# Performance work log

Measured on AMD Instinct MI355X. Metric: run time of the kernel, lower is better.

The kernel has to match this reference:

```python
import jax, jax.numpy as jnp
import numpy as np
from jax import lax

DIM = 192
HEADS = 4
K = 3
PAD = 1


def conv2d(x, w, groups=1, pad=0):
    # x: [B,C,H,W], w: [O, C//groups, kh, kw]
    return lax.conv_general_dilated(
        x, w, window_strides=(1, 1), padding=[(pad, pad), (pad, pad)],
        dimension_numbers=("NCHW", "OIHW", "NCHW"), feature_group_count=groups)


def setup_inputs() -> dict:
    key = jax.random.key(0)
    ks = jax.random.split(key, 8)
    b, c, h, w = 2, DIM, 256, 256
    x = jax.random.normal(ks[0], (b, c, h, w), dtype=jnp.float32)
    y = jax.random.normal(ks[1], (b, c, h, w), dtype=jnp.float32)
    s = 0.05
    qk_w = jax.random.normal(ks[2], (2 * DIM, DIM, 1, 1), dtype=jnp.float32) * s
    qk_dw_w = jax.random.normal(ks[3], (2 * DIM, 1, K, K), dtype=jnp.float32) * s  # depthwise, groups=2*dim
    v_w = jax.random.normal(ks[4], (DIM, DIM, 1, 1), dtype=jnp.float32) * s
    v_dw_w = jax.random.normal(ks[5], (DIM, DIM, K, K), dtype=jnp.float32) * s    # NOTE: not grouped in source
    proj_w = jax.random.normal(ks[6], (DIM, DIM, 1, 1), dtype=jnp.float32) * s
    temperature = jnp.ones((HEADS, 1, 1), dtype=jnp.float32)
    return {"x": x, "y": y, "qk_w": qk_w, "qk_dw_w": qk_dw_w, "v_w": v_w,
            "v_dw_w": v_dw_w, "proj_w": proj_w, "temperature": temperature}


def reference(x, y, qk_w, qk_dw_w, v_w, v_dw_w, proj_w, temperature):
    b, c, h, w = x.shape
    hd = c // HEADS  # channels per head
    qk = conv2d(conv2d(x, qk_w), qk_dw_w, groups=2 * DIM, pad=PAD)  # [b, 2c, h, w]
    q, k = jnp.split(qk, 2, axis=1)
    v = conv2d(conv2d(y, v_w), v_dw_w, pad=PAD)  # full conv (groups=1), per source

    def to_heads(t):
        return t.reshape(b, HEADS, hd, h * w)  # b head c (hw)

    q, k, v = to_heads(q), to_heads(k), to_heads(v)
    # L2 normalize along spatial (last) axis, eps matches torch F.normalize (1e-12)
    q = q / jnp.maximum(jnp.linalg.norm(q, axis=-1, keepdims=True), 1e-12)
    k = k / jnp.maximum(jnp.linalg.norm(k, axis=-1, keepdims=True), 1e-12)
    attn = jnp.einsum("bhcn,bhdn->bhcd", q, k) * temperature  # [b, head, c, c]
    attn = jax.nn.softmax(attn, axis=-1)
    out = jnp.einsum("bhcd,bhdn->bhcn", attn, v)
    out = out.reshape(b, c, h, w)
    return conv2d(out, proj_w)
```

## Files before the change

kernel.cpp:

```cpp
#include <hip/hip_runtime.h>
#include <hip/hip_bf16.h>

#define NPIX 65536
#define CDIM 192
#define C2   384
#define HEADS 4
#define HD   48
#define PROW 258
#define XTROWS (PROW * PROW)

typedef float f32x4 __attribute__((ext_vector_type(4)));
typedef short short8 __attribute__((ext_vector_type(8)));

__device__ __forceinline__ unsigned short f2bf(float x) {
  union { float f; unsigned u; } v; v.f = x;
  unsigned r = v.u + 0x7fff + ((v.u >> 16) & 1);
  return (unsigned short)(r >> 16);
}
__device__ __forceinline__ float bf2f(unsigned short x) {
  union { unsigned u; float f; } v; v.u = ((unsigned)x) << 16;
  return v.f;
}
__device__ __forceinline__ int f4(int r) { return (r ^ (r >> 2)) & 3; }

__device__ __forceinline__ void gload_lds16(const void* g, void* l) {
  __builtin_amdgcn_global_load_lds(
      (const __attribute__((address_space(1))) unsigned int*)g,
      (__attribute__((address_space(3))) unsigned int*)l, 16, 0, 0);
}

__global__ __launch_bounds__(256) void castw_kernel(
    const float* __restrict__ qkw, const float* __restrict__ vw,
    unsigned short* __restrict__ wqk, unsigned short* __restrict__ wv) {
  int i = blockIdx.x * 256 + threadIdx.x;
  if (i < C2 * CDIM) wqk[i] = f2bf(qkw[i]);
  if (i < CDIM * CDIM) wv[i] = f2bf(vw[i]);
}

__global__ __launch_bounds__(512) void qk_mfma_kernel(
    const float* __restrict__ X0, const unsigned short* __restrict__ W,
    unsigned short* __restrict__ Out0) {
  const int b = blockIdx.y;
  const float* X = X0 + (size_t)b * CDIM * NPIX;
  unsigned short* Out = Out0 + (size_t)b * C2 * NPIX;
  const int px0 = blockIdx.x * 128;
  __shared__ __align__(16) char smem[67584];
  short* sA = (short*)smem;
  short* sB = (short*)(smem + 49152);
  const int t = threadIdx.x;
  const int lane = t & 63;
  const int wid = t >> 6;
  const int cpp = t & 31;
  const int pg = t >> 5;
  const int l15 = lane & 15;
  const int l4 = lane >> 4;

  f32x4 acc[3][8];
#pragma unroll
  for (int mi = 0; mi < 3; ++mi)
#pragma unroll
    for (int ni = 0; ni < 8; ++ni) acc[mi][ni] = (f32x4){0.f, 0.f, 0.f, 0.f};

  for (int k0 = 0; k0 < CDIM; k0 += 64) {
#pragma unroll
    for (int i = 0; i < 6; ++i) {
      int g = i * 512 + t;
      int row = g >> 3, ck = g & 7;
      gload_lds16(W + (size_t)row * CDIM + k0 + ((ck ^ (row & 7)) * 8),
                  (char*)sA + ((size_t)i * 512 + (t & ~63)) * 16);
    }
    {
      const float* xp = X + (size_t)(k0 + 2 * cpp) * NPIX + px0 + 8 * pg;
      float4 a0 = *(const float4*)xp;
      float4 a1 = *(const float4*)(xp + 4);
      float4 b0 = *(const float4*)(xp + NPIX);
      float4 b1 = *(const float4*)(xp + NPIX + 4);
      float av[8] = {a0.x, a0.y, a0.z, a0.w, a1.x, a1.y, a1.z, a1.w};
      float bv[8] = {b0.x, b0.y, b0.z, b0.w, b1.x, b1.y, b1.z, b1.w};
#pragma unroll
      for (int i = 0; i < 8; ++i) {
        unsigned d = (unsigned)f2bf(av[i]) | ((unsigned)f2bf(bv[i]) << 16);
        *(unsigned*)&sB[(8 * pg + i) * 72 + 2 * cpp] = d;
      }
    }
    asm volatile("s_waitcnt vmcnt(0)");
    __syncthreads();
#pragma unroll
    for (int kk = 0; kk < 2; ++kk) {
      short8 af[3], bf[8];
#pragma unroll
      for (int mi = 0; mi < 3; ++mi) {
        int row = wid * 48 + mi * 16 + l15;
        af[mi] = *(const short8*)&sA[row * 64 +
                                     (((kk * 4 + l4) ^ (row & 7)) * 8)];
      }
#pragma unroll
      for (int ni = 0; ni < 8; ++ni)
        bf[ni] = *(const short8*)&sB[(ni * 16 + l15) * 72 + (kk * 4 + l4) * 8];
#pragma unroll
      for (int mi = 0; mi < 3; ++mi)
#pragma unroll
        for (int ni = 0; ni < 8; ++ni)
          acc[mi][ni] = __builtin_amdgcn_mfma_f32_16x16x32_bf16(
              af[mi], bf[ni], acc[mi][ni], 0, 0, 0);
    }
    __syncthreads();
  }
  short* zones = (short*)smem;
  short* zone = zones + wid * 2176;
#pragma unroll
  for (int mi = 0; mi < 3; ++mi) {
#pragma unroll
    for (int ni = 0; ni < 8; ++ni)
#pragma unroll
      for (int rg = 0; rg < 4; ++rg)
        zone[(l4 * 4 + rg) * 136 + ni * 16 + l15] =
            (short)f2bf(acc[mi][ni][rg]);
    asm volatile("s_waitcnt lgkmcnt(0)" ::: "memory");
    __builtin_amdgcn_sched_barrier(0);
#pragma unroll
    for (int it = 0; it < 4; ++it) {
      int e = it * 64 + lane;
      int ol = e >> 4, pxg = e & 15;
      short8 vv = *(const short8*)&zone[ol * 136 + pxg * 8];
      *(short8*)&Out[(size_t)(wid * 48 + mi * 16 + ol) * NPIX + px0 + pxg * 8] = vv;
    }
    asm volatile("s_waitcnt lgkmcnt(0)" ::: "memory");
    __builtin_amdgcn_sched_barrier(0);
  }
}

__global__ __launch_bounds__(256, 4) void v_mfma_kernel(
    const float* __restrict__ Y0, const unsigned short* __restrict__ W,
    unsigned short* __restrict__ Xt0) {
  const int b = blockIdx.y;
  const float* Y = Y0 + (size_t)b * CDIM * NPIX;
  unsigned short* Xt = Xt0 + (size_t)b * XTROWS * CDIM;
  const int px0 = blockIdx.x * 64;
  const int h = px0 >> 8;
  const int w0 = px0 & 255;
  __shared__ __align__(16) char smem[34816];
  const int t = threadIdx.x;
  const int lane = t & 63;
  const int wid = t >> 6;
  const int cp = t & 15;
  const int pg = t >> 4;
  const int l15 = lane & 15;
  const int l4 = lane >> 4;

  f32x4 acc[12];
#pragma unroll
  for (int ni = 0; ni < 12; ++ni) acc[ni] = (f32x4){0.f, 0.f, 0.f, 0.f};

#define SXB(p) ((short*)(smem + (p) * 5120))
#define SWB(p) ((short*)(smem + 10240 + (p) * 12288))

#define STAGE_W(k0_, p_)                                                     \
  {                                                                          \
    _Pragma("unroll")                                                        \
    for (int i = 0; i < 3; ++i) {                                            \
      int e = i * 256 + t;                                                   \
      int oc = e >> 2, kg = e & 3;                                           \
      gload_lds16(W + (size_t)oc * CDIM + (k0_) + (kg ^ f4(oc)) * 8,         \
                  (char*)SWB(p_) + ((size_t)i * 256 + (t & ~63)) * 16);      \
    }                                                                        \
  }

  float4 ya, yb;
#define LOAD_Y(k0_)                                                          \
  {                                                                          \
    const float* xp = Y + (size_t)((k0_) + 2 * cp) * NPIX + px0 + 4 * pg;    \
    ya = *(const float4*)xp;                                                 \
    yb = *(const float4*)(xp + NPIX);                                        \
  }
#define WRITE_X(p_)                                                          \
  {                                                                          \
    float av[4] = {ya.x, ya.y, ya.z, ya.w};                                  \
    float bv[4] = {yb.x, yb.y, yb.z, yb.w};                                  \
    short* sx = SXB(p_);                                                     \
    _Pragma("unroll")                                                        \
    for (int i = 0; i < 4; ++i) {                                            \
      unsigned d = (unsigned)f2bf(av[i]) | ((unsigned)f2bf(bv[i]) << 16);    \
      *(unsigned*)&sx[(4 * pg + i) * 40 + 2 * cp] = d;                       \
    }                                                                        \
  }

  LOAD_Y(0);
  STAGE_W(0, 0);
  WRITE_X(0);
  asm volatile("s_waitcnt vmcnt(0)" ::: "memory");
  __syncthreads();

  for (int k = 0; k < 6; ++k) {
    const int p = k & 1;
    if (k < 5) {
      LOAD_Y((k + 1) * 32);
      STAGE_W((k + 1) * 32, p ^ 1);
    }
    {
      short* sx = SXB(p);
      short* sw = SWB(p);
      short8 af = *(const short8*)&sx[(wid * 16 + l15) * 40 + l4 * 8];
      short8 bf[12];
#pragma unroll
      for (int ni = 0; ni < 12; ++ni) {
        int row = ni * 16 + l15;
        bf[ni] = *(const short8*)&sw[row * 32 + (l4 ^ f4(row)) * 8];
      }
#pragma unroll
      for (int ni = 0; ni < 12; ++ni)
        acc[ni] = __builtin_amdgcn_mfma_f32_16x16x32_bf16(af, bf[ni], acc[ni],
                                                          0, 0, 0);
    }
    if (k < 5) WRITE_X(p ^ 1);
    asm volatile("s_waitcnt vmcnt(0)" ::: "memory");
    __syncthreads();
  }
#undef STAGE_W
#undef LOAD_Y
#undef WRITE_X
#undef SXB
#undef SWB

  short* zone = (short*)(smem + 10240) + wid * (16 * 104);
#pragma unroll
  for (int oh = 0; oh < 2; ++oh) {
#pragma unroll
    for (int ni = 0; ni < 6; ++ni)
#pragma unroll
      for (int rg = 0; rg < 4; ++rg)
        zone[(l4 * 4 + rg) * 104 + ni * 16 + l15] =
            (short)f2bf(acc[oh * 6 + ni][rg]);
    asm volatile("s_waitcnt lgkmcnt(0)" ::: "memory");
    __builtin_amdgcn_sched_barrier(0);
#pragma unroll
    for (int it = 0; it < 3; ++it) {
      int e = it * 64 + lane;
      int pl = e / 12, cg = e % 12;
      short8 vv = *(const short8*)&zone[pl * 104 + cg * 8];
      size_t xrow = (size_t)(h + 1) * PROW + (w0 + wid * 16 + pl + 1);
      *(short8*)&Xt[xrow * CDIM + oh * 96 + cg * 8] = vv;
    }
    asm volatile("s_waitcnt lgkmcnt(0)" ::: "memory");
    __builtin_amdgcn_sched_barrier(0);
  }
}

__global__ __launch_bounds__(128) void border_zero_kernel(
    unsigned short* __restrict__ Xt0) {
  unsigned short* Xt = Xt0 + (size_t)blockIdx.y * XTROWS * CDIM;
  int pos = blockIdx.x;
  size_t row;
  if (pos < 258) row = pos;
  else if (pos < 516) row = (size_t)257 * PROW + (pos - 258);
  else { int i = pos - 516; row = (size_t)(1 + (i >> 1)) * PROW + ((i & 1) ? 257 : 0); }
  unsigned* p = (unsigned*)(Xt + row * CDIM);
  if (threadIdx.x < 96) p[threadIdx.x] = 0;
}

__global__ __launch_bounds__(256) void dwgram_kernel(
    const unsigned short* __restrict__ qkb0, const float* __restrict__ dw,
    float* __restrict__ gpart, float* __restrict__ ssp) {
  const int head = blockIdx.y;
  const int b = blockIdx.z;
  const int bh = b * HEADS + head;
  const unsigned short* qkb = qkb0 + (size_t)b * C2 * NPIX;
  float* gpart_b = gpart + (size_t)bh * 64 * (HD * HD);
  float* ssp_b = ssp + (size_t)bh * 64 * 96;
  const int braw = blockIdx.x;
  const int blk = (braw & 7) * 8 + (braw >> 3);
  const int t = threadIdx.x;
  const int lane = t & 63;
  const int wid = t >> 6;

  __shared__ __align__(16) char smem[38400];
  short* zone = (short*)smem + wid * (96 * 40);

  const int qrow0 = HD * head, krow0 = CDIM + HD * head;
  const int p0 = (lane & 1) * 16;
  const int c0 = (lane >> 1) * 3;

  float wr[3][9];
#pragma unroll
  for (int j = 0; j < 3; ++j) {
    int ch = c0 + j;
    int srow = (ch < HD) ? (qrow0 + ch) : (krow0 + ch - HD);
#pragma unroll
    for (int i = 0; i < 9; ++i) wr[j][i] = dw[srow * 9 + i];
  }

  f32x4 acc[3][3];
#pragma unroll
  for (int mi = 0; mi < 3; ++mi)
#pragma unroll
    for (int nj = 0; nj < 3; ++nj) acc[mi][nj] = (f32x4){0.f, 0.f, 0.f, 0.f};
  float ss[3] = {0.f, 0.f, 0.f};

  const int hr = blk * 4 + wid;
  for (int s = 0; s < 8; ++s) {
    const int col0 = s * 32;
    const int cl = col0 + p0;
#pragma unroll
    for (int j = 0; j < 3; ++j) {
      int ch = c0 + j;
      int srow = (ch < HD) ? (qrow0 + ch) : (krow0 + ch - HD);
      const unsigned short* ip = qkb + (size_t)srow * NPIX;
      float win[3][18];
#pragma unroll
      for (int r = 0; r < 3; ++r) {
        int ir = hr - 1 + r;
        if ((unsigned)ir < 256u) {
          const unsigned short* rp = ip + ir * 256 + cl;
          short8 v0 = *(const short8*)rp;
          short8 v1 = *(const short8*)(rp + 8);
#pragma unroll
          for (int q = 0; q < 8; ++q) {
            win[r][1 + q] = bf2f((unsigned short)v0[q]);
            win[r][9 + q] = bf2f((unsigned short)v1[q]);
          }
          win[r][0]  = (cl > 0)        ? bf2f(rp[-1]) : 0.f;
          win[r][17] = (cl + 16 < 256) ? bf2f(rp[16]) : 0.f;
        } else {
#pragma unroll
          for (int q = 0; q < 18; ++q) win[r][q] = 0.f;
        }
      }
      unsigned pk[8];
#pragma unroll
      for (int p = 0; p < 16; ++p) {
        float sacc = 0.f;
#pragma unroll
        for (int r = 0; r < 3; ++r)
#pragma unroll
          for (int c = 0; c < 3; ++c) sacc += wr[j][r * 3 + c] * win[r][p + c];
        ss[j] += sacc * sacc;
        unsigned short bb = f2bf(sacc);
        if (p & 1) pk[p >> 1] |= ((unsigned)bb << 16);
        else       pk[p >> 1] = bb;
      }
      unsigned* zp = (unsigned*)&zone[ch * 40 + p0];
#pragma unroll
      for (int q = 0; q < 8; ++q) zp[q] = pk[q];
    }
    asm volatile("s_waitcnt lgkmcnt(0)" ::: "memory");
    __builtin_amdgcn_sched_barrier(0);
    short8 qf[3], kf[3];
#pragma unroll
    for (int mi = 0; mi < 3; ++mi)
      qf[mi] = *(const short8*)&zone[(mi * 16 + (lane & 15)) * 40 +
                                     (lane >> 4) * 8];
#pragma unroll
    for (int nj = 0; nj < 3; ++nj)
      kf[nj] = *(const short8*)&zone[(HD + nj * 16 + (lane & 15)) * 40 +
                                     (lane >> 4) * 8];
#pragma unroll
    for (int mi = 0; mi < 3; ++mi)
#pragma unroll
      for (int nj = 0; nj < 3; ++nj)
        acc[mi][nj] = __builtin_amdgcn_mfma_f32_16x16x32_bf16(
            qf[mi], kf[nj], acc[mi][nj], 0, 0, 0);
    asm volatile("s_waitcnt lgkmcnt(0)" ::: "memory");
    __builtin_amdgcn_sched_barrier(0);
  }
  __syncthreads();
  float* red   = (float*)smem;
  float* ssred = (float*)(smem + 36864);
#pragma unroll
  for (int mi = 0; mi < 3; ++mi)
#pragma unroll
    for (int nj = 0; nj < 3; ++nj) {
      int kj = nj * 16 + (lane & 15);
#pragma unroll
      for (int rg = 0; rg < 4; ++rg) {
        int qi = mi * 16 + (lane >> 4) * 4 + rg;
        red[wid * 2304 + qi * HD + kj] = acc[mi][nj][rg];
      }
    }
#pragma unroll
  for (int j = 0; j < 3; ++j) {
    float sj = ss[j] + __shfl_xor(ss[j], 1);
    if ((lane & 1) == 0) ssred[wid * 96 + c0 + j] = sj;
  }
  __syncthreads();
  float* gp = gpart_b + (size_t)blk * (HD * HD);
  for (int e = t; e < HD * HD; e += 256)
    gp[e] = red[e] + red[2304 + e] + red[4608 + e] + red[6912 + e];
  if (t < 96)
    ssp_b[(size_t)blk * 96 + t] =
        ssred[t] + ssred[96 + t] + ssred[192 + t] + ssred[288 + t];
}

__global__ __launch_bounds__(64) void normred_kernel(
    const float* __restrict__ ssp, float* __restrict__ norms) {
  int idx = blockIdx.x;
  int bh = idx / 96, ch = idx % 96;
  int l = threadIdx.x;
  float s = ssp[((size_t)bh * 64 + l) * 96 + ch];
#pragma unroll
  for (int off = 32; off; off >>= 1) s += __shfl_down(s, off);
  if (l == 0) {
    int b = bh >> 2, hh = bh & 3;
    int g = b * C2 + (ch < HD ? hh * HD + ch : CDIM + hh * HD + ch - HD);
    norms[g] = sqrtf(s);
  }
}

__global__ __launch_bounds__(256) void gramred_kernel(
    const float* __restrict__ part, float* __restrict__ logits) {
  int ij = blockIdx.x * 256 + threadIdx.x;
  int bh = blockIdx.y;
  if (ij >= HD * HD) return;
  const float* pp = part + (size_t)bh * 64 * (HD * HD);
  float s = 0.f;
  for (int sp = 0; sp < 64; ++sp) s += pp[(size_t)sp * (HD * HD) + ij];
  logits[(size_t)bh * (HD * HD) + ij] = s;
}

__global__ __launch_bounds__(64) void softmax_kernel(
    float* __restrict__ logits, const float* __restrict__ norms,
    const float* __restrict__ temperature) {
  int hh = blockIdx.x, b = blockIdx.y;
  int i = threadIdx.x;
  if (i >= HD) return;
  const float eps = 1e-12f;
  float temp = temperature[hh];
  float nq = fmaxf(norms[b * C2 + HD * hh + i], eps);
  float* row = logits + (((size_t)b * HEADS + hh) * HD + i) * HD;
  float vals[48];
  float mx = -1e30f;
#pragma unroll
  for (int j = 0; j < HD; ++j) {
    float nk = fmaxf(norms[b * C2 + CDIM + HD * hh + j], eps);
    float v = row[j] / (nq * nk) * temp;
    vals[j] = v;
    mx = fmaxf(mx, v);
  }
  float sum = 0.f;
#pragma unroll
  for (int j = 0; j < HD; ++j) {
    vals[j] = expf(vals[j] - mx);
    sum += vals[j];
  }
  float inv = 1.f / sum;
#pragma unroll
  for (int j = 0; j < HD; ++j) row[j] = vals[j] * inv;
}

__global__ __launch_bounds__(256) void buildM_kernel(
    const float* __restrict__ attn, const float* __restrict__ projw,
    float* __restrict__ M) {
  int idx = blockIdx.x * 256 + threadIdx.x;
  if (idx >= 2 * CDIM * CDIM) return;
  int d = idx % CDIM;
  int oc = (idx / CDIM) % CDIM;
  int b = idx / (CDIM * CDIM);
  int hh = d / HD, dd = d % HD;
  const float* arow = attn + ((size_t)b * HEADS + hh) * HD * HD;
  float s = 0.f;
#pragma unroll
  for (int c = 0; c < HD; ++c)
    s += projw[oc * CDIM + HD * hh + c] * arow[c * HD + dd];
  M[idx] = s;
}

__global__ __launch_bounds__(256) void wtrans_kernel(
    const float* __restrict__ M, const float* __restrict__ Wv,
    unsigned short* __restrict__ Wb) {
  const int ocb = blockIdx.x * 4;
  const int ec0 = blockIdx.y * 432;
  const int b = blockIdx.z;
  __shared__ float sM[4][CDIM];
  for (int i = threadIdx.x; i < 4 * CDIM; i += 256)
    sM[i / CDIM][i % CDIM] =
        M[((size_t)b * CDIM + ocb + i / CDIM) * CDIM + (i % CDIM)];
  __syncthreads();
  for (int e = ec0 + threadIdx.x; e < ec0 + 432; e += 256) {
    float a0 = 0.f, a1 = 0.f, a2 = 0.f, a3 = 0.f;
#pragma unroll 4
    for (int d = 0; d < CDIM; ++d) {
      float wv = Wv[(size_t)d * (CDIM * 9) + e];
      a0 += sM[0][d] * wv; a1 += sM[1][d] * wv;
      a2 += sM[2][d] * wv; a3 += sM[3][d] * wv;
    }
    int ic = e / 9, tap = e % 9;
    size_t base = (((size_t)b * 9 + tap) * CDIM) * CDIM + ic;
    Wb[base + (size_t)(ocb + 0) * CDIM] = f2bf(a0);
    Wb[base + (size_t)(ocb + 1) * CDIM] = f2bf(a1);
    Wb[base + (size_t)(ocb + 2) * CDIM] = f2bf(a2);
    Wb[base + (size_t)(ocb + 3) * CDIM] = f2bf(a3);
  }
}

__global__ __launch_bounds__(256, 3) void conv3x3_mfma_kernel(
    const unsigned short* __restrict__ XtAll,
    const unsigned short* __restrict__ WbAll,
    float* __restrict__ outAll) {
  const int bb = blockIdx.y;
  const unsigned short* Xt = XtAll + (size_t)bb * XTROWS * CDIM;
  const unsigned short* Wb = WbAll + (size_t)bb * 9 * CDIM * CDIM;
  float* out = outAll + (size_t)bb * CDIM * NPIX;

  const int d = blockIdx.x;
  const int xcd = d & 7;
  const int j = d >> 3;
  const int h = xcd * 32 + j / 3;
  const int oc0 = (j % 3) * 64;

  __shared__ __align__(16) short sA[3 * 64 * 32];
  __shared__ __align__(16) short sB[2][258 * 32];

  const int t = threadIdx.x;
  const int lane = t & 63;
  const int wid = t >> 6;
  const int l15 = lane & 15;
  const int l4 = lane >> 4;

  f32x4 acc[4][4];
#pragma unroll
  for (int mi = 0; mi < 4; ++mi)
#pragma unroll
    for (int ni = 0; ni < 4; ++ni) acc[mi][ni] = (f32x4){0.f, 0.f, 0.f, 0.f};

#define STAGE_A(sidx)                                                        \
  {                                                                          \
    const int ra_ = (sidx) / 6;                                              \
    const int ica_ = ((sidx) % 6) * 32;                                      \
    _Pragma("unroll")                                                        \
    for (int i = 0; i < 3; ++i) {                                            \
      int g = i * 256 + t;                                                   \
      int row = g >> 2, ck = g & 3;                                          \
      int tap = row >> 6, oc = row & 63;                                     \
      gload_lds16(Wb + ((size_t)(ra_ * 3 + tap) * CDIM + oc0 + oc) * CDIM +  \
                      ica_ + (ck ^ f4(row)) * 8,                             \
                  (char*)sA + (size_t)(i * 256 + wid * 64) * 16);            \
    }                                                                        \
  }
#define STAGE_B(sidx, bi)                                                    \
  {                                                                          \
    const int rs_ = (sidx) / 6;                                              \
    const int ics_ = ((sidx) % 6) * 32;                                      \
    const unsigned short* bsrc =                                             \
        Xt + (size_t)(h + rs_) * PROW * CDIM + ics_;                         \
    _Pragma("unroll")                                                        \
    for (int i = 0; i < 4; ++i) {                                            \
      int g = i * 256 + t;                                                   \
      int row = g >> 2, ck = g & 3;                                          \
      gload_lds16(bsrc + (size_t)row * CDIM + (ck ^ f4(row)) * 8,            \
                  (char*)sB[bi] + (size_t)(i * 256 + wid * 64) * 16);        \
    }                                                                        \
    { int g = 1024 + wid * 2 + lane;                                         \
      int row = g >> 2, ck = g & 3;                                          \
      if (lane < 2)                                                          \
        gload_lds16(bsrc + (size_t)row * CDIM + (ck ^ f4(row)) * 8,          \
                    (char*)sB[bi] + (size_t)(1024 + wid * 2) * 16);          \
    }                                                                        \
  }

  STAGE_A(0);
  STAGE_B(0, 0);
  asm volatile("s_waitcnt vmcnt(0)" ::: "memory");
  __syncthreads();

  int cur = 0;
  for (int s = 0; s < 18; ++s) {
    short8 af_[3][4];
#pragma unroll
    for (int c = 0; c < 3; ++c)
#pragma unroll
      for (int mi = 0; mi < 4; ++mi) {
        int row = c * 64 + mi * 16 + l15;
        af_[c][mi] = *(const short8*)&sA[row * 32 + (l4 ^ f4(row)) * 8];
      }
    __syncthreads();
    if (s < 17) {
      STAGE_A(s + 1);
      STAGE_B(s + 1, cur ^ 1);
    }
#pragma unroll
    for (int c = 0; c < 3; ++c) {
      short8 bf[4];
#pragma unroll
      for (int ni = 0; ni < 4; ++ni) {
        int row = wid * 64 + ni * 16 + l15 + c;
        bf[ni] = *(const short8*)&sB[cur][row * 32 + (l4 ^ f4(row)) * 8];
      }
#pragma unroll
      for (int mi = 0; mi < 4; ++mi)
#pragma unroll
        for (int ni = 0; ni < 4; ++ni)
          acc[mi][ni] = __builtin_amdgcn_mfma_f32_16x16x32_bf16(
              af_[c][mi], bf[ni], acc[mi][ni], 0, 0, 0);
    }
    asm volatile("s_waitcnt vmcnt(0)" ::: "memory");
    __syncthreads();
    cur ^= 1;
  }
#undef STAGE_A
#undef STAGE_B
#pragma unroll
  for (int mi = 0; mi < 4; ++mi) {
    int ocl = oc0 + mi * 16 + l4 * 4;
#pragma unroll
    for (int ni = 0; ni < 4; ++ni) {
      int wloc = wid * 64 + ni * 16 + l15;
#pragma unroll
      for (int rg = 0; rg < 4; ++rg)
        out[(size_t)(ocl + rg) * NPIX + h * 256 + wloc] = acc[mi][ni][rg];
    }
  }
}

extern "C" void kernel_launch(void* const* d_in, const int* in_sizes, int n_in,
                              void* d_out, int out_size, void* d_ws, size_t ws_size,
                              hipStream_t stream) {
  const float* x          = (const float*)d_in[0];
  const float* y          = (const float*)d_in[1];
  const float* qk_w       = (const float*)d_in[2];
  const float* qk_dw_w    = (const float*)d_in[3];
  const float* v_w        = (const float*)d_in[4];
  const float* v_dw_w     = (const float*)d_in[5];
  const float* proj_w     = (const float*)d_in[6];
  const float* temperature= (const float*)d_in[7];
  float* out = (float*)d_out;

  unsigned short* qkb = (unsigned short*)d_ws;
  unsigned short* XtA = qkb;
  float* gpart  = (float*)(qkb + (size_t)2 * C2 * NPIX);
  float* ssp    = gpart + (size_t)8 * 64 * HD * HD;
  float* norms  = ssp + (size_t)8 * 64 * 96;
  float* logits = norms + 768;
  float* M      = logits + 2 * HEADS * HD * HD;
  unsigned short* wqk = (unsigned short*)(M + 2 * CDIM * CDIM);
  unsigned short* wv  = wqk + C2 * CDIM;
  unsigned short* Wb  = wv + CDIM * CDIM;
  size_t needB = (size_t)((char*)(Wb + (size_t)2 * 9 * CDIM * CDIM) - (char*)d_ws);
  if (ws_size < needB) return;

  castw_kernel<<<dim3(288), dim3(256), 0, stream>>>(qk_w, v_w, wqk, wv);

  qk_mfma_kernel<<<dim3(512, 2), dim3(512), 0, stream>>>(x, wqk, qkb);
  dwgram_kernel<<<dim3(64, HEADS, 2), dim3(256), 0, stream>>>(
      qkb, qk_dw_w, gpart, ssp);
  normred_kernel<<<dim3(768), dim3(64), 0, stream>>>(ssp, norms);
  gramred_kernel<<<dim3(9, 8), dim3(256), 0, stream>>>(gpart, logits);
  softmax_kernel<<<dim3(4, 2), dim3(64), 0, stream>>>(logits, norms, temperature);
  buildM_kernel<<<dim3(288), dim3(256), 0, stream>>>(logits, proj_w, M);
  wtrans_kernel<<<dim3(48, 4, 2), dim3(256), 0, stream>>>(M, v_dw_w, Wb);

  border_zero_kernel<<<dim3(1028, 2), dim3(128), 0, stream>>>(XtA);
  v_mfma_kernel<<<dim3(1024, 2), dim3(256), 0, stream>>>(y, wv, XtA);
  conv3x3_mfma_kernel<<<dim3(768, 2), dim3(256), 0, stream>>>(XtA, Wb, out);
}
```

Baseline: 342.0 us.

## Merge dwgram, v projection and border zeroing into one launch

Combines the depthwise-conv/Gram kernel, the v 1x1 projection MFMA kernel and the border-zero kernel into a single launch that dispatches on block index. The workspace is re-laid out so XtA no longer aliases qkb, which allows the v projection to run concurrently with the dwgram work and fill the machine better. In exchange the workspace grows, the launch bound of 4 on the v path is dropped, and the fused kernel is limited by the register use of the heavier branch.

```diff
diff --git a/kernel.cpp b/kernel.cpp
--- a/kernel.cpp
+++ b/kernel.cpp
@@ -130,264 +130,263 @@
   }
 }
 
-__global__ __launch_bounds__(256, 4) void v_mfma_kernel(
-    const float* __restrict__ Y0, const unsigned short* __restrict__ W,
+__global__ __launch_bounds__(256) void dwgram_v_kernel(
+    const unsigned short* __restrict__ qkb0, const float* __restrict__ dw,
+    float* __restrict__ gpart, float* __restrict__ ssp,
+    const float* __restrict__ Y0, const unsigned short* __restrict__ Wv,
     unsigned short* __restrict__ Xt0) {
-  const int b = blockIdx.y;
-  const float* Y = Y0 + (size_t)b * CDIM * NPIX;
-  unsigned short* Xt = Xt0 + (size_t)b * XTROWS * CDIM;
-  const int px0 = blockIdx.x * 64;
-  const int h = px0 >> 8;
-  const int w0 = px0 & 255;
-  __shared__ __align__(16) char smem[34816];
+  __shared__ __align__(16) char smem[38400];
   const int t = threadIdx.x;
   const int lane = t & 63;
   const int wid = t >> 6;
-  const int cp = t & 15;
-  const int pg = t >> 4;
   const int l15 = lane & 15;
   const int l4 = lane >> 4;
 
-  f32x4 acc[12];
-#pragma unroll
-  for (int ni = 0; ni < 12; ++ni) acc[ni] = (f32x4){0.f, 0.f, 0.f, 0.f};
+  if (blockIdx.x < 512) {
+    const int idx = blockIdx.x;
+    const int braw = idx & 63;
+    const int head = (idx >> 6) & 3;
+    const int b = idx >> 8;
+    const int bh = b * HEADS + head;
+    const unsigned short* qkb = qkb0 + (size_t)b * C2 * NPIX;
+    float* gpart_b = gpart + (size_t)bh * 64 * (HD * HD);
+    float* ssp_b = ssp + (size_t)bh * 64 * 96;
+    const int blk = (braw & 7) * 8 + (braw >> 3);
+
+    short* zone = (short*)smem + wid * (96 * 40);
+
+    const int qrow0 = HD * head, krow0 = CDIM + HD * head;
+    const int p0 = (lane & 1) * 16;
+    const int c0 = (lane >> 1) * 3;
+
+    float wr[3][9];
+#pragma unroll
+    for (int j = 0; j < 3; ++j) {
+      int ch = c0 + j;
+      int srow = (ch < HD) ? (qrow0 + ch) : (krow0 + ch - HD);
+#pragma unroll
+      for (int i = 0; i < 9; ++i) wr[j][i] = dw[srow * 9 + i];
+    }
+
+    f32x4 acc[3][3];
+#pragma unroll
+    for (int mi = 0; mi < 3; ++mi)
+#pragma unroll
+      for (int nj = 0; nj < 3; ++nj) acc[mi][nj] = (f32x4){0.f, 0.f, 0.f, 0.f};
+    float ss[3] = {0.f, 0.f, 0.f};
+
+    const int hr = blk * 4 + wid;
+    for (int s = 0; s < 8; ++s) {
+      const int cl = s * 32 + p0;
+#pragma unroll
+      for (int j = 0; j < 3; ++j) {
+        int ch = c0 + j;
+        int srow = (ch < HD) ? (qrow0 + ch) : (krow0 + ch - HD);
+        const unsigned short* ip = qkb + (size_t)srow * NPIX;
+        float win[3][18];
+#pragma unroll
+        for (int r = 0; r < 3; ++r) {
+          int ir = hr - 1 + r;
+          if ((unsigned)ir < 256u) {
+            const unsigned short* rp = ip + ir * 256 + cl;
+            short8 v0 = *(const short8*)rp;
+            short8 v1 = *(const short8*)(rp + 8);
+#pragma unroll
+            for (int q = 0; q < 8; ++q) {
+              win[r][1 + q] = bf2f((unsigned short)v0[q]);
+              win[r][9 + q] = bf2f((unsigned short)v1[q]);
+            }
+            win[r][0]  = (cl > 0)        ? bf2f(rp[-1]) : 0.f;
+            win[r][17] = (cl + 16 < 256) ? bf2f(rp[16]) : 0.f;
+          } else {
+#pragma unroll
+            for (int q = 0; q < 18; ++q) win[r][q] = 0.f;
+          }
+        }
+        unsigned pk[8];
+#pragma unroll
+        for (int p = 0; p < 16; ++p) {
+          float sacc = 0.f;
+#pragma unroll
+          for (int r = 0; r < 3; ++r)
+#pragma unroll
+            for (int c = 0; c < 3; ++c) sacc += wr[j][r * 3 + c] * win[r][p + c];
+          ss[j] += sacc * sacc;
+          unsigned short bb = f2bf(sacc);
+          if (p & 1) pk[p >> 1] |= ((unsigned)bb << 16);
+          else       pk[p >> 1] = bb;
+        }
+        unsigned* zp = (unsigned*)&zone[ch * 40 + p0];
+#pragma unroll
+        for (int q = 0; q < 8; ++q) zp[q] = pk[q];
+      }
+      asm volatile("s_waitcnt lgkmcnt(0)" ::: "memory");
+      __builtin_amdgcn_sched_barrier(0);
+      short8 qf[3], kf[3];
+#pragma unroll
+      for (int mi = 0; mi < 3; ++mi)
+        qf[mi] = *(const short8*)&zone[(mi * 16 + l15) * 40 + l4 * 8];
+#pragma unroll
+      for (int nj = 0; nj < 3; ++nj)
+        kf[nj] = *(const short8*)&zone[(HD + nj * 16 + l15) * 40 + l4 * 8];
+#pragma unroll
+      for (int mi = 0; mi < 3; ++mi)
+#pragma unroll
+        for (int nj = 0; nj < 3; ++nj)
+          acc[mi][nj] = __builtin_amdgcn_mfma_f32_16x16x32_bf16(
+              qf[mi], kf[nj], acc[mi][nj], 0, 0, 0);
+      asm volatile("s_waitcnt lgkmcnt(0)" ::: "memory");
+      __builtin_amdgcn_sched_barrier(0);
+    }
+    __syncthreads();
+    float* red   = (float*)smem;
+    float* ssred = (float*)(smem + 36864);
+#pragma unroll
+    for (int mi = 0; mi < 3; ++mi)
+#pragma unroll
+      for (int nj = 0; nj < 3; ++nj) {
+        int kj = nj * 16 + l15;
+#pragma unroll
+        for (int rg = 0; rg < 4; ++rg) {
+          int qi = mi * 16 + l4 * 4 + rg;
+          red[wid * 2304 + qi * HD + kj] = acc[mi][nj][rg];
+        }
+      }
+#pragma unroll
+    for (int j = 0; j < 3; ++j) {
+      float sj = ss[j] + __shfl_xor(ss[j], 1);
+      if ((lane & 1) == 0) ssred[wid * 96 + c0 + j] = sj;
+    }
+    __syncthreads();
+    float* gp = gpart_b + (size_t)blk * (HD * HD);
+    for (int e = t; e < HD * HD; e += 256)
+      gp[e] = red[e] + red[2304 + e] + red[4608 + e] + red[6912 + e];
+    if (t < 96)
+      ssp_b[(size_t)blk * 96 + t] =
+          ssred[t] + ssred[96 + t] + ssred[192 + t] + ssred[288 + t];
+    return;
+  }
+
+  if (blockIdx.x < 2560) {
+    const int idx = blockIdx.x - 512;
+    const int b = idx >> 10;
+    const float* Y = Y0 + (size_t)b * CDIM * NPIX;
+    unsigned short* Xt = Xt0 + (size_t)b * XTROWS * CDIM;
+    const int px0 = (idx & 1023) * 64;
+    const int h = px0 >> 8;
+    const int w0 = px0 & 255;
+    const int cp = t & 15;
+    const int pg = t >> 4;
+
+    f32x4 acc[12];
+#pragma unroll
+    for (int ni = 0; ni < 12; ++ni) acc[ni] = (f32x4){0.f, 0.f, 0.f, 0.f};
 
 #define SXB(p) ((short*)(smem + (p) * 5120))
 #define SWB(p) ((short*)(smem + 10240 + (p) * 12288))
-
 #define STAGE_W(k0_, p_)                                                     \
-  {                                                                          \
-    _Pragma("unroll")                                                        \
-    for (int i = 0; i < 3; ++i) {                                            \
-      int e = i * 256 + t;                                                   \
-      int oc = e >> 2, kg = e & 3;                                           \
-      gload_lds16(W + (size_t)oc * CDIM + (k0_) + (kg ^ f4(oc)) * 8,         \
-                  (char*)SWB(p_) + ((size_t)i * 256 + (t & ~63)) * 16);      \
-    }                                                                        \
-  }
-
-  float4 ya, yb;
+    {                                                                        \
+      _Pragma("unroll")                                                      \
+      for (int i = 0; i < 3; ++i) {                                          \
+        int e = i * 256 + t;                                                 \
+        int oc = e >> 2, kg = e & 3;                                         \
+        gload_lds16(Wv + (size_t)oc * CDIM + (k0_) + (kg ^ f4(oc)) * 8,      \
+                    (char*)SWB(p_) + ((size_t)i * 256 + (t & ~63)) * 16);    \
+      }                                                                      \
+    }
+    float4 ya, yb;
 #define LOAD_Y(k0_)                                                          \
-  {                                                                          \
-    const float* xp = Y + (size_t)((k0_) + 2 * cp) * NPIX + px0 + 4 * pg;    \
-    ya = *(const float4*)xp;                                                 \
-    yb = *(const float4*)(xp + NPIX);                                        \
-  }
+    {                                                                        \
+      const float* xp = Y + (size_t)((k0_) + 2 * cp) * NPIX + px0 + 4 * pg;  \
+      ya = *(const float4*)xp;                                               \
+      yb = *(const float4*)(xp + NPIX);                                      \
+    }
 #define WRITE_X(p_)                                                          \
-  {                                                                          \
-    float av[4] = {ya.x, ya.y, ya.z, ya.w};                                  \
-    float bv[4] = {yb.x, yb.y, yb.z, yb.w};                                  \
-    short* sx = SXB(p_);                                                     \
-    _Pragma("unroll")                                                        \
-    for (int i = 0; i < 4; ++i) {                                            \
-      unsigned d = (unsigned)f2bf(av[i]) | ((unsigned)f2bf(bv[i]) << 16);    \
-      *(unsigned*)&sx[(4 * pg + i) * 40 + 2 * cp] = d;                       \
-    }                                                                        \
-  }
-
-  LOAD_Y(0);
-  STAGE_W(0, 0);
-  WRITE_X(0);
-  asm volatile("s_waitcnt vmcnt(0)" ::: "memory");
-  __syncthreads();
-
-  for (int k = 0; k < 6; ++k) {
-    const int p = k & 1;
-    if (k < 5) {
-      LOAD_Y((k + 1) * 32);
-      STAGE_W((k + 1) * 32, p ^ 1);
-    }
-    {
-      short* sx = SXB(p);
-      short* sw = SWB(p);
-      short8 af = *(const short8*)&sx[(wid * 16 + l15) * 40 + l4 * 8];
-      short8 bf[12];
-#pragma unroll
-      for (int ni = 0; ni < 12; ++ni) {
-        int row = ni * 16 + l15;
-        bf[ni] = *(const short8*)&sw[row * 32 + (l4 ^ f4(row)) * 8];
-      }
-#pragma unroll
-      for (int ni = 0; ni < 12; ++ni)
-        acc[ni] = __builtin_amdgcn_mfma_f32_16x16x32_bf16(af, bf[ni], acc[ni],
-                                                          0, 0, 0);
-    }
-    if (k < 5) WRITE_X(p ^ 1);
+    {                                                                        \
+      float av[4] = {ya.x, ya.y, ya.z, ya.w};                                \
+      float bv[4] = {yb.x, yb.y, yb.z, yb.w};                                \
+      short* sx = SXB(p_);                                                   \
+      _Pragma("unroll")                                                      \
+      for (int i = 0; i < 4; ++i) {                                          \
+        unsigned d = (unsigned)f2bf(av[i]) | ((unsigned)f2bf(bv[i]) << 16);  \
+        *(unsigned*)&sx[(4 * pg + i) * 40 + 2 * cp] = d;                     \
+      }                                                                      \
+    }
+
+    LOAD_Y(0);
+    STAGE_W(0, 0);
+    WRITE_X(0);
     asm volatile("s_waitcnt vmcnt(0)" ::: "memory");
     __syncthreads();
-  }
+
+    for (int k = 0; k < 6; ++k) {
+      const int p = k & 1;
+      if (k < 5) {
+        LOAD_Y((k + 1) * 32);
+        STAGE_W((k + 1) * 32, p ^ 1);
+      }
+      {
+        short* sx = SXB(p);
+        short* sw = SWB(p);
+        short8 af = *(const short8*)&sx[(wid * 16 + l15) * 40 + l4 * 8];
+        short8 bf[12];
+#pragma unroll
+        for (int ni = 0; ni < 12; ++ni) {
+          int row = ni * 16 + l15;
+          bf[ni] = *(const short8*)&sw[row * 32 + (l4 ^ f4(row)) * 8];
+        }
+#pragma unroll
+        for (int ni = 0; ni < 12; ++ni)
+          acc[ni] = __builtin_amdgcn_mfma_f32_16x16x32_bf16(af, bf[ni], acc[ni],
+                                                            0, 0, 0);
+      }
+      if (k < 5) WRITE_X(p ^ 1);
+      asm volatile("s_waitcnt vmcnt(0)" ::: "memory");
+      __syncthreads();
+    }
 #undef STAGE_W
 #undef LOAD_Y
 #undef WRITE_X
 #undef SXB
 #undef SWB
 
-  short* zone = (short*)(smem + 10240) + wid * (16 * 104);
-#pragma unroll
-  for (int oh = 0; oh < 2; ++oh) {
-#pragma unroll
-    for (int ni = 0; ni < 6; ++ni)
-#pragma unroll
-      for (int rg = 0; rg < 4; ++rg)
-        zone[(l4 * 4 + rg) * 104 + ni * 16 + l15] =
-            (short)f2bf(acc[oh * 6 + ni][rg]);
-    asm volatile("s_waitcnt lgkmcnt(0)" ::: "memory");
-    __builtin_amdgcn_sched_barrier(0);
-#pragma unroll
-    for (int it = 0; it < 3; ++it) {
-      int e = it * 64 + lane;
-      int pl = e / 12, cg = e % 12;
-      short8 vv = *(const short8*)&zone[pl * 104 + cg * 8];
-      size_t xrow = (size_t)(h + 1) * PROW + (w0 + wid * 16 + pl + 1);
-      *(short8*)&Xt[xrow * CDIM + oh * 96 + cg * 8] = vv;
-    }
-    asm volatile("s_waitcnt lgkmcnt(0)" ::: "memory");
-    __builtin_amdgcn_sched_barrier(0);
-  }
-}
-
-__global__ __launch_bounds__(128) void border_zero_kernel(
-    unsigned short* __restrict__ Xt0) {
-  unsigned short* Xt = Xt0 + (size_t)blockIdx.y * XTROWS * CDIM;
-  int pos = blockIdx.x;
-  size_t row;
-  if (pos < 258) row = pos;
-  else if (pos < 516) row = (size_t)257 * PROW + (pos - 258);
-  else { int i = pos - 516; row = (size_t)(1 + (i >> 1)) * PROW + ((i & 1) ? 257 : 0); }
-  unsigned* p = (unsigned*)(Xt + row * CDIM);
-  if (threadIdx.x < 96) p[threadIdx.x] = 0;
-}
-
-__global__ __launch_bounds__(256) void dwgram_kernel(
-    const unsigned short* __restrict__ qkb0, const float* __restrict__ dw,
-    float* __restrict__ gpart, float* __restrict__ ssp) {
-  const int head = blockIdx.y;
-  const int b = blockIdx.z;
-  const int bh = b * HEADS + head;
-  const unsigned short* qkb = qkb0 + (size_t)b * C2 * NPIX;
-  float* gpart_b = gpart + (size_t)bh * 64 * (HD * HD);
-  float* ssp_b = ssp + (size_t)bh * 64 * 96;
-  const int braw = blockIdx.x;
-  const int blk = (braw & 7) * 8 + (braw >> 3);
-  const int t = threadIdx.x;
-  const int lane = t & 63;
-  const int wid = t >> 6;
-
-  __shared__ __align__(16) char smem[38400];
-  short* zone = (short*)smem + wid * (96 * 40);
-
-  const int qrow0 = HD * head, krow0 = CDIM + HD * head;
-  const int p0 = (lane & 1) * 16;
-  const int c0 = (lane >> 1) * 3;
-
-  float wr[3][9];
-#pragma unroll
-  for (int j = 0; j < 3; ++j) {
-    int ch = c0 + j;
-    int srow = (ch < HD) ? (qrow0 + ch) : (krow0 + ch - HD);
-#pragma unroll
-    for (int i = 0; i < 9; ++i) wr[j][i] = dw[srow * 9 + i];
-  }
-
-  f32x4 acc[3][3];
-#pragma unroll
-  for (int mi = 0; mi < 3; ++mi)
-#pragma unroll
-    for (int nj = 0; nj < 3; ++nj) acc[mi][nj] = (f32x4){0.f, 0.f, 0.f, 0.f};
-  float ss[3] = {0.f, 0.f, 0.f};
-
-  const int hr = blk * 4 + wid;
-  for (int s = 0; s < 8; ++s) {
-    const int col0 = s * 32;
-    const int cl = col0 + p0;
-#pragma unroll
-    for (int j = 0; j < 3; ++j) {
-      int ch = c0 + j;
-      int srow = (ch < HD) ? (qrow0 + ch) : (krow0 + ch - HD);
-      const unsigned short* ip = qkb + (size_t)srow * NPIX;
-      float win[3][18];
-#pragma unroll
-      for (int r = 0; r < 3; ++r) {
-        int ir = hr - 1 + r;
-        if ((unsigned)ir < 256u) {
-          const unsigned short* rp = ip + ir * 256 + cl;
-          short8 v0 = *(const short8*)rp;
-          short8 v1 = *(const short8*)(rp + 8);
-#pragma unroll
-          for (int q = 0; q < 8; ++q) {
-            win[r][1 + q] = bf2f((unsigned short)v0[q]);
-            win[r][9 + q] = bf2f((unsigned short)v1[q]);
-          }
-          win[r][0]  = (cl > 0)        ? bf2f(rp[-1]) : 0.f;
-          win[r][17] = (cl + 16 < 256) ? bf2f(rp[16]) : 0.f;
-        } else {
-#pragma unroll
-          for (int q = 0; q < 18; ++q) win[r][q] = 0.f;
-        }
-      }
-      unsigned pk[8];
-#pragma unroll
-      for (int p = 0; p < 16; ++p) {
-        float sacc = 0.f;
-#pragma unroll
-        for (int r = 0; r < 3; ++r)
-#pragma unroll
-          for (int c = 0; c < 3; ++c) sacc += wr[j][r * 3 + c] * win[r][p + c];
-        ss[j] += sacc * sacc;
-        unsigned short bb = f2bf(sacc);
-        if (p & 1) pk[p >> 1] |= ((unsigned)bb << 16);
-        else       pk[p >> 1] = bb;
-      }
-      unsigned* zp = (unsigned*)&zone[ch * 40 + p0];
-#pragma unroll
-      for (int q = 0; q < 8; ++q) zp[q] = pk[q];
-    }
-    asm volatile("s_waitcnt lgkmcnt(0)" ::: "memory");
-    __builtin_amdgcn_sched_barrier(0);
-    short8 qf[3], kf[3];
-#pragma unroll
-    for (int mi = 0; mi < 3; ++mi)
-      qf[mi] = *(const short8*)&zone[(mi * 16 + (lane & 15)) * 40 +
-                                     (lane >> 4) * 8];
-#pragma unroll
-    for (int nj = 0; nj < 3; ++nj)
-      kf[nj] = *(const short8*)&zone[(HD + nj * 16 + (lane & 15)) * 40 +
-                                     (lane >> 4) * 8];
-#pragma unroll
-    for (int mi = 0; mi < 3; ++mi)
-#pragma unroll
-      for (int nj = 0; nj < 3; ++nj)
-        acc[mi][nj] = __builtin_amdgcn_mfma_f32_16x16x32_bf16(
-            qf[mi], kf[nj], acc[mi][nj], 0, 0, 0);
-    asm volatile("s_waitcnt lgkmcnt(0)" ::: "memory");
-    __builtin_amdgcn_sched_barrier(0);
-  }
-  __syncthreads();
-  float* red   = (float*)smem;
-  float* ssred = (float*)(smem + 36864);
-#pragma unroll
-  for (int mi = 0; mi < 3; ++mi)
-#pragma unroll
-    for (int nj = 0; nj < 3; ++nj) {
-      int kj = nj * 16 + (lane & 15);
-#pragma unroll
-      for (int rg = 0; rg < 4; ++rg) {
-        int qi = mi * 16 + (lane >> 4) * 4 + rg;
-        red[wid * 2304 + qi * HD + kj] = acc[mi][nj][rg];
-      }
-    }
-#pragma unroll
-  for (int j = 0; j < 3; ++j) {
-    float sj = ss[j] + __shfl_xor(ss[j], 1);
-    if ((lane & 1) == 0) ssred[wid * 96 + c0 + j] = sj;
-  }
-  __syncthreads();
-  float* gp = gpart_b + (size_t)blk * (HD * HD);
-  for (int e = t; e < HD * HD; e += 256)
-    gp[e] = red[e] + red[2304 + e] + red[4608 + e] + red[6912 + e];
-  if (t < 96)
-    ssp_b[(size_t)blk * 96 + t] =
-        ssred[t] + ssred[96 + t] + ssred[192 + t] + ssred[288 + t];
+    short* zone = (short*)(smem + 10240) + wid * (16 * 104);
+#pragma unroll
+    for (int oh = 0; oh < 2; ++oh) {
+#pragma unroll
+      for (int ni = 0; ni < 6; ++ni)
+#pragma unroll
+        for (int rg = 0; rg < 4; ++rg)
+          zone[(l4 * 4 + rg) * 104 + ni * 16 + l15] =
+              (short)f2bf(acc[oh * 6 + ni][rg]);
+      asm volatile("s_waitcnt lgkmcnt(0)" ::: "memory");
+      __builtin_amdgcn_sched_barrier(0);
+#pragma unroll
+      for (int it = 0; it < 3; ++it) {
+        int e = it * 64 + lane;
+        int pl = e / 12, cg = e % 12;
+        short8 vv = *(const short8*)&zone[pl * 104 + cg * 8];
+        size_t xrow = (size_t)(h + 1) * PROW + (w0 + wid * 16 + pl + 1);
+        *(short8*)&Xt[xrow * CDIM + oh * 96 + cg * 8] = vv;
+      }
+      asm volatile("s_waitcnt lgkmcnt(0)" ::: "memory");
+      __builtin_amdgcn_sched_barrier(0);
+    }
+    return;
+  }
+
+  {
+    const int pos = blockIdx.x - 2560;
+    const int b = t >> 7;
+    const int tl = t & 127;
+    unsigned short* Xt = Xt0 + (size_t)b * XTROWS * CDIM;
+    size_t row;
+    if (pos < 258) row = pos;
+    else if (pos < 516) row = (size_t)257 * PROW + (pos - 258);
+    else { int i = pos - 516; row = (size_t)(1 + (i >> 1)) * PROW + ((i & 1) ? 257 : 0); }
+    unsigned* p = (unsigned*)(Xt + row * CDIM);
+    if (tl < 96) p[tl] = 0;
+  }
 }
 
 __global__ __launch_bounds__(64) void normred_kernel(
@@ -624,8 +623,8 @@
   float* out = (float*)d_out;
 
   unsigned short* qkb = (unsigned short*)d_ws;
-  unsigned short* XtA = qkb;
-  float* gpart  = (float*)(qkb + (size_t)2 * C2 * NPIX);
+  unsigned short* XtA = qkb + (size_t)2 * C2 * NPIX;
+  float* gpart  = (float*)(XtA + (size_t)2 * XTROWS * CDIM);
   float* ssp    = gpart + (size_t)8 * 64 * HD * HD;
   float* norms  = ssp + (size_t)8 * 64 * 96;
   float* logits = norms + 768;
@@ -639,15 +638,15 @@
   castw_kernel<<<dim3(288), dim3(256), 0, stream>>>(qk_w, v_w, wqk, wv);
 
   qk_mfma_kernel<<<dim3(512, 2), dim3(512), 0, stream>>>(x, wqk, qkb);
-  dwgram_kernel<<<dim3(64, HEADS, 2), dim3(256), 0, stream>>>(
-      qkb, qk_dw_w, gpart, ssp);
+
+  dwgram_v_kernel<<<dim3(3588), dim3(256), 0, stream>>>(
+      qkb, qk_dw_w, gpart, ssp, y, wv, XtA);
+
   normred_kernel<<<dim3(768), dim3(64), 0, stream>>>(ssp, norms);
   gramred_kernel<<<dim3(9, 8), dim3(256), 0, stream>>>(gpart, logits);
   softmax_kernel<<<dim3(4, 2), dim3(64), 0, stream>>>(logits, norms, temperature);
   buildM_kernel<<<dim3(288), dim3(256), 0, stream>>>(logits, proj_w, M);
   wtrans_kernel<<<dim3(48, 4, 2), dim3(256), 0, stream>>>(M, v_dw_w, Wb);
 
-  border_zero_kernel<<<dim3(1028, 2), dim3(128), 0, stream>>>(XtA);
-  v_mfma_kernel<<<dim3(1024, 2), dim3(256), 0, stream>>>(y, wv, XtA);
   conv3x3_mfma_kernel<<<dim3(768, 2), dim3(256), 0, stream>>>(XtA, Wb, out);
 }
```

Result: no change. 345.4 us (+1.0%).
